# Kernel tuning notes

Measured on AMD Instinct MI355X. Metric: run time of the kernel, lower is better.

The kernel has to match this reference:

```python
import jax, jax.numpy as jnp
import numpy as np

N_BATCH = 2; N_RAYS = 4096; S_COARSE = 32; S_FINE = 32
FEATURE_DIM = 32; BOX_WARP = 6.0; EPS = 1e-5

_PLANE_AXES = np.array([[[1, 0, 0], [0, 1, 0], [0, 0, 1]],
                        [[1, 0, 0], [0, 0, 1], [0, 1, 0]],
                        [[0, 0, 1], [0, 1, 0], [1, 0, 0]]], dtype=np.float32)
_INV_PLANES = np.linalg.inv(_PLANE_AXES)  # [3,3,3]


def _grid_sample(feat, coords):
    # feat [B,C,H,W], coords [B,M,2] in [-1,1] (x->W, y->H); bilinear, align_corners=False, zero padding
    B, C, H, W = feat.shape
    x = (coords[..., 0] + 1.0) * (W * 0.5) - 0.5
    y = (coords[..., 1] + 1.0) * (H * 0.5) - 0.5
    x0 = jnp.floor(x); y0 = jnp.floor(y)
    wx = x - x0; wy = y - y0
    x0i = x0.astype(jnp.int32); y0i = y0.astype(jnp.int32)

    def corner(fb, yi, xi):
        valid = ((xi >= 0) & (xi < W) & (yi >= 0) & (yi < H)).astype(fb.dtype)
        v = fb[:, jnp.clip(yi, 0, H - 1), jnp.clip(xi, 0, W - 1)]  # [C,M]
        return v * valid[None, :]

    def one(fb, x0b, y0b, wxb, wyb):
        x1b = x0b + 1; y1b = y0b + 1
        return (corner(fb, y0b, x0b) * (1 - wxb) * (1 - wyb)
                + corner(fb, y0b, x1b) * wxb * (1 - wyb)
                + corner(fb, y1b, x0b) * (1 - wxb) * wyb
                + corner(fb, y1b, x1b) * wxb * wyb)  # [C,M]

    return jax.vmap(one)(feat, x0i, y0i, wx, wy)  # [B,C,M]


def _sample_from_planes(planes, coords):
    # planes [N,3,C,H,W], coords [N,M,3] -> [N,3,M,C]
    N, n_planes, C, H, W = planes.shape
    M = coords.shape[1]
    c = coords * (2.0 / BOX_WARP)
    proj = jnp.einsum('nmc,pcd->npmd', c, jnp.asarray(_INV_PLANES))[..., :2]  # [N,3,M,2]
    out = _grid_sample(planes.reshape(N * n_planes, C, H, W), proj.reshape(N * n_planes, M, 2))
    return out.reshape(N, n_planes, C, M).transpose(0, 1, 3, 2)


def _decoder(feat, W1, b1, W2, b2):
    # OSGDecoder: Linear -> softplus -> Linear; rgb sigmoid-squashed, sigma raw
    h = jax.nn.softplus(feat @ W1 + b1)
    o = h @ W2 + b2
    rgb = jax.nn.sigmoid(o[..., 1:]) * (1 + 2 * 0.001) - 0.001
    sigma = o[..., 0:1]
    return rgb, sigma


def _run_model(planes, coords, W1, b1, W2, b2, beta):
    sf = _sample_from_planes(planes, coords).mean(axis=1)  # [N,M,C]
    rgb, raw_sigma = _decoder(sf, W1, b1, W2, b2)
    pred_sdf = raw_sigma
    # template SDF stand-in (external FLAME tex_feature net): sphere SDF
    tsdf = jnp.linalg.norm(coords, axis=-1, keepdims=True) - 0.5
    sigma = raw_sigma + tsdf
    density = jax.nn.sigmoid(-sigma / beta) / beta  # sdf_activation(-sigma)
    return rgb, density, pred_sdf


def _ray_march(colors, densities, depths):
    deltas = depths[:, :, 1:] - depths[:, :, :-1]
    c_mid = 0.5 * (colors[:, :, :-1] + colors[:, :, 1:])
    d_mid = 0.5 * (densities[:, :, :-1] + densities[:, :, 1:])
    z_mid = 0.5 * (depths[:, :, :-1] + depths[:, :, 1:])
    alpha = 1.0 - jnp.exp(-d_mid * deltas)
    shifted = jnp.concatenate([jnp.ones_like(alpha[:, :, :1]), 1.0 - alpha + 1e-10], axis=2)
    weights = alpha * jnp.cumprod(shifted, axis=2)[:, :, :-1]
    comp_rgb = jnp.sum(weights * c_mid, axis=2) * 2.0 - 1.0
    w_tot = jnp.sum(weights, axis=2)
    comp_depth = jnp.sum(weights * z_mid, axis=2) / w_tot
    comp_depth = jnp.nan_to_num(comp_depth, nan=jnp.inf)
    comp_depth = jnp.clip(comp_depth, depths.min(), depths.max())
    return comp_rgb, comp_depth, weights


def _sample_pdf(bins, weights, u):
    n_w = weights.shape[-1]
    w = weights + EPS
    pdf = w / jnp.sum(w, axis=-1, keepdims=True)
    cdf = jnp.cumsum(pdf, axis=-1)
    cdf = jnp.concatenate([jnp.zeros_like(cdf[:, :1]), cdf], axis=-1)
    inds = jax.vmap(lambda c, uu: jnp.searchsorted(c, uu, side='right'))(cdf, u)
    below = jnp.maximum(inds - 1, 0)
    above = jnp.minimum(inds, n_w)
    cdf0 = jnp.take_along_axis(cdf, below, axis=-1)
    cdf1 = jnp.take_along_axis(cdf, above, axis=-1)
    b0 = jnp.take_along_axis(bins, below, axis=-1)
    b1v = jnp.take_along_axis(bins, above, axis=-1)
    denom = cdf1 - cdf0
    denom = jnp.where(denom < EPS, 1.0, denom)
    return b0 + (u - cdf0) / denom * (b1v - b0)


def _sample_importance(z_vals, weights, u):
    B, R, S, _ = z_vals.shape
    z = z_vals.reshape(B * R, S)
    w = weights.reshape(B * R, -1)  # S-1
    # torch max_pool1d(k=2,s=1,pad=1) then avg_pool1d(k=2,s=1)
    neg = jnp.full_like(w[:, :1], -1e10)
    wp = jnp.concatenate([neg, w, neg], axis=-1)
    m = jnp.maximum(wp[:, :-1], wp[:, 1:])  # len S
    w_sm = 0.5 * (m[:, :-1] + m[:, 1:]) + 0.01  # len S-1
    z_mid = 0.5 * (z[:, :-1] + z[:, 1:])  # len S-1
    s = _sample_pdf(z_mid, w_sm[:, 1:-1], u)
    return jax.lax.stop_gradient(s.reshape(B, R, -1, 1))


def reference(planes, ray_origins, ray_directions, hit_min_depth, hit_max_depth, jitter, u_importance, W1, b1, W2, b2, sigmoid_beta, hit_mask):
    N, M, _ = ray_origins.shape
    beta = jnp.maximum(sigmoid_beta, 0.002)
    mask = hit_mask.astype(planes.dtype)[:, :, None, None]  # [N,M,1,1]
    hmin = jnp.where(mask == 0, hit_min_depth.min(), hit_min_depth)
    hmax = jnp.where(mask == 0, hit_max_depth.max(), hit_max_depth)
    base = jnp.linspace(0.0, 1.0, S_COARSE, dtype=planes.dtype).reshape(1, 1, S_COARSE, 1)
    span = hmax - hmin
    d_coarse = (base + jitter * span / S_COARSE) * span + hmin  # [N,M,S,1]

    def eval_points(depths):
        coords = ray_origins[:, :, None, :] + depths * ray_directions[:, :, None, :]
        S = depths.shape[2]
        rgb, dens, psdf = _run_model(planes, coords.reshape(N, M * S, 3), W1, b1, W2, b2, beta)
        # masked scatter-back into dense buffers == multiply by hit mask
        rgb = rgb.reshape(N, M, S, FEATURE_DIM) * mask
        dens = dens.reshape(N, M, S, 1) * mask
        return rgb, dens, psdf

    rgb_c, dens_c, psdf_c = eval_points(d_coarse)
    _, _, w_c = _ray_march(rgb_c, dens_c, d_coarse)
    d_fine = _sample_importance(d_coarse, w_c, u_importance)
    rgb_f, dens_f, psdf_f = eval_points(d_fine)

    all_d = jnp.concatenate([d_coarse, d_fine], axis=2)
    all_c = jnp.concatenate([rgb_c, rgb_f], axis=2)
    all_s = jnp.concatenate([dens_c, dens_f], axis=2)
    idx = jnp.argsort(all_d, axis=2)
    all_d = jnp.take_along_axis(all_d, idx, axis=2)
    all_c = jnp.take_along_axis(all_c, jnp.broadcast_to(idx, all_c.shape), axis=2)
    all_s = jnp.take_along_axis(all_s, jnp.broadcast_to(idx, all_s.shape), axis=2)

    rgb_final, depth_final, weights = _ray_march(all_c, all_s, all_d)
    all_pred_sdf = jnp.concatenate([psdf_c, psdf_f], axis=1)
    return rgb_final, depth_final, weights, all_pred_sdf


def setup_inputs():
    key = jax.random.key(0)
    ks = jax.random.split(key, 12)
    planes = jax.random.normal(ks[0], (N_BATCH, 3, 32, 256, 256), jnp.float32)
    ray_origins = 0.1 * jax.random.normal(ks[1], (N_BATCH, N_RAYS, 3), jnp.float32)
    rd = jax.random.normal(ks[2], (N_BATCH, N_RAYS, 3), jnp.float32)
    ray_directions = rd / jnp.linalg.norm(rd, axis=-1, keepdims=True)
    hit_min_depth = 0.8 + 0.4 * jax.random.uniform(ks[3], (N_BATCH, N_RAYS, 1, 1), jnp.float32)
    hit_max_depth = hit_min_depth + 0.5 + jax.random.uniform(ks[4], (N_BATCH, N_RAYS, 1, 1), jnp.float32)
    jitter = jax.random.uniform(ks[5], (N_BATCH, N_RAYS, S_COARSE, 1), jnp.float32)
    u_importance = jax.random.uniform(ks[6], (N_BATCH * N_RAYS, S_FINE), jnp.float32)
    W1 = 0.05 * jax.random.normal(ks[7], (32, 64), jnp.float32)
    b1 = jnp.zeros((64,), jnp.float32)
    W2 = 0.05 * jax.random.normal(ks[8], (64, 1 + FEATURE_DIM), jnp.float32)
    b2 = jnp.zeros((1 + FEATURE_DIM,), jnp.float32)
    sigmoid_beta = 0.1 * jnp.ones((1,), jnp.float32)
    hit_mask = jax.random.randint(ks[9], (N_BATCH, N_RAYS), 0, 2, jnp.int32)
    return {'planes': planes, 'ray_origins': ray_origins, 'ray_directions': ray_directions,
            'hit_min_depth': hit_min_depth, 'hit_max_depth': hit_max_depth, 'jitter': jitter,
            'u_importance': u_importance, 'W1': W1, 'b1': b1, 'W2': W2, 'b2': b2,
            'sigmoid_beta': sigmoid_beta, 'hit_mask': hit_mask}
```

## Files before the change

### kernel.cpp

```cpp
#include <hip/hip_runtime.h>
#include <hip/hip_bf16.h>
#include <math.h>
#include <stddef.h>

typedef unsigned int u32;
typedef unsigned short u16;
typedef unsigned long long u64;

#define NRAYS 8192
#define NSAMP 262144

__device__ __forceinline__ float fa(float a,float b){ return __fadd_rn(a,b); }
__device__ __forceinline__ float fs(float a,float b){ return __fsub_rn(a,b); }
__device__ __forceinline__ float fm(float a,float b){ return __fmul_rn(a,b); }
__device__ __forceinline__ float fdv(float a,float b){ return __fdiv_rn(a,b); }

__device__ __forceinline__ double exp_d(double x){
  const double LOG2E  = 1.4426950408889634074;
  const double LN2_HI = 6.93147180369123816490e-01;
  const double LN2_LO = 1.90821492927058770002e-10;
  double kd = rint(x * LOG2E);
  if (kd >  200.0) return INFINITY;
  if (kd < -200.0) return 0.0;
  int k = (int)kd;
  double r = fma(-kd, LN2_HI, x);
  r = fma(-kd, LN2_LO, r);
  double p = 1.0/39916800.0;
  p = fma(p, r, 1.0/3628800.0);
  p = fma(p, r, 1.0/362880.0);
  p = fma(p, r, 1.0/40320.0);
  p = fma(p, r, 1.0/5040.0);
  p = fma(p, r, 1.0/720.0);
  p = fma(p, r, 1.0/120.0);
  p = fma(p, r, 1.0/24.0);
  p = fma(p, r, 1.0/6.0);
  p = fma(p, r, 0.5);
  p = fma(p, r, 1.0);
  p = fma(p, r, 1.0);
  u64 sb = ((u64)(k + 1023)) << 52;
  return p * __longlong_as_double((long long)sb);
}
__device__ __forceinline__ float exf(float x){ return (float)exp_d((double)x); }
__device__ __forceinline__ float sigm(float x){
  if (x >= 0.f){ float e = exf(-x); return fdv(1.f, fa(1.f, e)); }
  float e = exf(x); return fdv(e, fa(1.f, e));
}
__device__ __forceinline__ float sigm_fast(float x){
  return 1.f/(1.f + __expf(-x));
}
__device__ __forceinline__ u16 f2b(float f){
  u32 x = __float_as_uint(f);
  return (u16)((x + 0x7fffu + ((x>>16)&1u)) >> 16);
}
__device__ __forceinline__ u32 fenc(float f){ u32 b=__float_as_uint(f); return (b&0x80000000u)? ~b : (b|0x80000000u); }
__device__ __forceinline__ float fdec(u32 k){ u32 b=(k&0x80000000u)? (k^0x80000000u) : ~k; return __uint_as_float(b); }

__global__ void k_init(const float* __restrict__ hmin, const float* __restrict__ hmax,
                       const float* __restrict__ W1, float* __restrict__ scal,
                       float* __restrict__ W1t){
  __shared__ float smn[256], smx[256];
  int t = threadIdx.x;
  float mn = 1e30f, mx = -1e30f;
  for (int i=t;i<NRAYS;i+=256){ mn=fminf(mn,hmin[i]); mx=fmaxf(mx,hmax[i]); }
  smn[t]=mn; smx[t]=mx; __syncthreads();
  for(int s=128;s>0;s>>=1){
    if(t<s){ smn[t]=fminf(smn[t],smn[t+s]); smx[t]=fmaxf(smx[t],smx[t+s]); }
    __syncthreads();
  }
  if(t==0){
    scal[0]=smn[0]; scal[1]=smx[0];
    ((u32*)scal)[2]=0xFFFFFFFFu;
    ((u32*)scal)[3]=0u;
  }
  for(int i=t;i<2048;i+=256){ int j=i>>5, c=i&31; W1t[i]=W1[c*64+j]; }
}

__global__ void __launch_bounds__(256) k_tr(const float* __restrict__ pl, float* __restrict__ pt){
  int t = blockIdx.x*256 + threadIdx.x;
  int x  = t & 255;
  int c4 = ((t>>8)&7)<<2;
  int y  = (t>>11)&255;
  int np = t>>19;
  const float* ip = pl + (((size_t)(np*32+c4))<<16) + (y<<8) + x;
  float4 o;
  o.x = ip[0];
  o.y = ip[65536];
  o.z = ip[131072];
  o.w = ip[196608];
  *reinterpret_cast<float4*>(pt + ((((size_t)(np<<8|y))<<8|x)<<5) + c4) = o;
}

template<int PHASE>
__global__ void __launch_bounds__(256) k_eval(
  const float* __restrict__ pt, const float* __restrict__ ro, const float* __restrict__ rd,
  const float* __restrict__ hmin, const float* __restrict__ hmax,
  const float* __restrict__ jitter, const int* __restrict__ hitmask,
  const float* __restrict__ W1t, const float* __restrict__ b1,
  const float* __restrict__ W2, const float* __restrict__ b2,
  const float* __restrict__ sb, float* __restrict__ scal,
  float* __restrict__ dep, float* __restrict__ dens_out, u16* __restrict__ rgb_out,
  float* __restrict__ out_psdf)
{
  __shared__ float sfeat[4][64][33];
  int tid = threadIdx.x;
  int wid = tid>>6, lane = tid&63;
  int blockbase = blockIdx.x*256;
  int idx = blockbase + tid;
  int ray = idx >> 5;
  int s   = idx & 31;
  int n   = ray >> 12;
  int msk = hitmask[ray];

  float d;
  if (PHASE==0){
    float hmn = msk ? hmin[ray] : scal[0];
    float hmx = msk ? hmax[ray] : scal[1];
    float span = fs(hmx, hmn);
    float jit  = jitter[idx];
    float base = (float)((double)s * (1.0/31.0));
    if (s==31) base = 1.0f;
    float t1 = fdv(fm(jit, span), 32.0f);
    d = fa(fm(fa(base, t1), span), hmn);
    dep[idx] = d;
    float dm=d, dM=d;
#pragma unroll
    for (int m=1;m<64;m<<=1){ dm=fminf(dm,__shfl_xor(dm,m)); dM=fmaxf(dM,__shfl_xor(dM,m)); }
    if ((tid & 63)==0){
      atomicMin(((u32*)scal)+2, fenc(dm));
      atomicMax(((u32*)scal)+3, fenc(dM));
    }
  } else {
    d = dep[idx];
  }

  float tsdf, cxo, cyo, czo;
  {
    const float sc2 = (float)(2.0/6.0);
    float ox=ro[ray*3+0], oy=ro[ray*3+1], oz=ro[ray*3+2];
    float dx=rd[ray*3+0], dy=rd[ray*3+1], dz=rd[ray*3+2];
    float px = fa(ox, fm(d,dx)), py = fa(oy, fm(d,dy)), pz = fa(oz, fm(d,dz));
    float nrm = __fsqrt_rn(fa(fa(fm(px,px),fm(py,py)),fm(pz,pz)));
    tsdf = fs(nrm, 0.5f);
    cxo = fm(px,sc2);
    cyo = fm(py,sc2);
    czo = fm(pz,sc2);
  }

  int pg = lane >> 3;
  int q  = lane & 7;
#pragma unroll 2
  for (int r=0;r<8;r++){
    int pidx = r*8 + pg;
    int n2   = ((blockbase + (wid<<6) + pidx) >> 17);
    float cx = __shfl(cxo, pidx);
    float cy = __shfl(cyo, pidx);
    float cz = __shfl(czo, pidx);

    float fchunk[4];
#pragma unroll
    for(int i=0;i<4;i++) fchunk[i]=0.f;

#pragma unroll
    for (int p=0;p<3;p++){
      float u = (p==2)?cz:cx;
      float v = (p==1)?cz:cy;
      float fx = fs(fm(fa(u,1.f),128.f),0.5f);
      float fy = fs(fm(fa(v,1.f),128.f),0.5f);
      float x0f = floorf(fx), y0f = floorf(fy);
      float wx = fs(fx,x0f), wy = fs(fy,y0f);
      float ax0 = fs(1.f,wx), ax1 = wx, ay0 = fs(1.f,wy), ay1 = wy;
      int x0, y0;
      {
        x0 = (x0f >= 2.1e9f) ? 2147483647 : ((x0f <= -2.1e9f) ? (-2147483647-1) : (int)x0f);
        y0 = (y0f >= 2.1e9f) ? 2147483647 : ((y0f <= -2.1e9f) ? (-2147483647-1) : (int)y0f);
      }
      int x1=x0+1, y1=y0+1;
      bool vx0 = (x0>=0 && x0<256), vx1 = (x1>=0 && x1<256);
      bool vy0 = (y0>=0 && y0<256), vy1 = (y1>=0 && y1<256);
      bool ok00 = vx0&&vy0, ok01 = vx1&&vy0, ok10 = vx0&&vy1, ok11 = vx1&&vy1;
      int cx0=min(max(x0,0),255), cx1=min(max(x1,0),255);
      int cy0=min(max(y0,0),255), cy1=min(max(y1,0),255);
      size_t pb = ((size_t)(n2*3+p))<<16;
      int qo = q<<2;
      const float4* t00 = (const float4*)(pt + ((pb + (cy0<<8) + cx0)<<5) + qo);
      const float4* t01 = (const float4*)(pt + ((pb + (cy0<<8) + cx1)<<5) + qo);
      const float4* t10 = (const float4*)(pt + ((pb + (cy1<<8) + cx0)<<5) + qo);
      const float4* t11 = (const float4*)(pt + ((pb + (cy1<<8) + cx1)<<5) + qo);
      float4 v00 = *t00, v01 = *t01, v10 = *t10, v11 = *t11;
      float e0,e1,e2,e3, t_;
#define CORNER_SUM(FLD, OUTI) \
      e0 = ok00 ? v00.FLD : 0.f; e1 = ok01 ? v01.FLD : 0.f; \
      e2 = ok10 ? v10.FLD : 0.f; e3 = ok11 ? v11.FLD : 0.f; \
      t_ = fa(fa(fa(fm(fm(e0,ax0),ay0), fm(fm(e1,ax1),ay0)), fm(fm(e2,ax0),ay1)), fm(fm(e3,ax1),ay1)); \
      fchunk[OUTI] = fa(fchunk[OUTI], t_);
      CORNER_SUM(x,0) CORNER_SUM(y,1) CORNER_SUM(z,2) CORNER_SUM(w,3)
#undef CORNER_SUM
    }
#pragma unroll
    for(int i=0;i<4;i++)
      sfeat[wid][pidx][q*4+i] = fdv(fchunk[i], 3.0f);
  }
  __syncthreads();

  float feat[32];
#pragma unroll
  for(int c=0;c<32;c++) feat[c] = sfeat[wid][lane][c];

  float o[33];
#pragma unroll
  for(int k=0;k<33;k++) o[k]=0.f;
#pragma unroll 2
  for(int j=0;j<64;j++){
    float a = 0.f;
#pragma unroll
    for(int c=0;c<32;c++) a = fmaf(feat[c], W1t[j*32+c], a);
    a = fa(a, b1[j]);
    float h = fa(fmaxf(a,0.f), __logf(fa(1.f, __expf(-fabsf(a)))));
#pragma unroll
    for(int k=0;k<33;k++) o[k] = fmaf(h, W2[j*33+k], o[k]);
  }
#pragma unroll
  for(int k=0;k<33;k++) o[k] = fa(o[k], b2[k]);

  float beta = fmaxf(sb[0], 0.002f);
  float raw = o[0];
  out_psdf[((size_t)n<<18) + ((size_t)PHASE<<17) + (size_t)(ray&4095)*32 + s] = raw;
  float sg = fa(raw, tsdf);
  float dens = msk ? fdv(sigm(fdv(-sg, beta)), beta) : 0.f;
  dens_out[idx]=dens;

  u16 rv[32];
#pragma unroll
  for(int c=0;c<32;c++){
    float r = msk ? fs(fm(sigm_fast(o[c+1]), 1.002f), 0.001f) : 0.f;
    rv[c]=f2b(r);
  }
  uint4* op = (uint4*)(rgb_out + (size_t)idx*32);
#pragma unroll
  for(int q2=0;q2<4;q2++){
    uint4 w;
    w.x = (u32)rv[q2*8+0] | ((u32)rv[q2*8+1]<<16);
    w.y = (u32)rv[q2*8+2] | ((u32)rv[q2*8+3]<<16);
    w.z = (u32)rv[q2*8+4] | ((u32)rv[q2*8+5]<<16);
    w.w = (u32)rv[q2*8+6] | ((u32)rv[q2*8+7]<<16);
    op[q2]=w;
  }
}

__global__ void __launch_bounds__(64) k_imp(
  const float* __restrict__ dc, const float* __restrict__ dens,
  const float* __restrict__ u_imp, float* __restrict__ df, float* __restrict__ scal)
{
  __shared__ float scdf[64][30];
  __shared__ float szm [64][30];
  int tid = threadIdx.x;
  int ray = blockIdx.x*64 + tid;
  float w[31];
  float dprev = dc[ray*32+0];
  float sprev = dens[ray*32+0];
  float T = 1.f;
#pragma unroll
  for(int i=0;i<31;i++){
    float dn = dc[ray*32+i+1];
    float sn = dens[ray*32+i+1];
    if (i<30) szm[tid][i] = fm(0.5f, fa(dprev,dn));
    float delta = fs(dn,dprev);
    float dm = fm(0.5f, fa(sprev,sn));
    float al = fs(1.f, exf(-fm(dm,delta)));
    w[i] = fm(al,T);
    T = fm(T, fa(fs(1.f,al), 1e-10f));
    dprev=dn; sprev=sn;
  }
  float pdfw[29];
#pragma unroll
  for(int i=0;i<29;i++){
    float m1 = fmaxf(w[i],w[i+1]), m2 = fmaxf(w[i+1],w[i+2]);
    pdfw[i] = fa(fa(fm(0.5f, fa(m1,m2)), 0.01f), 1e-5f);
  }
  float sum;
  {
    float r[8];
#pragma unroll
    for(int j=0;j<8;j++) r[j]=pdfw[j];
#pragma unroll
    for(int j=0;j<8;j++) r[j]=fa(r[j],pdfw[8+j]);
#pragma unroll
    for(int j=0;j<8;j++) r[j]=fa(r[j],pdfw[16+j]);
    sum = fa(fa(fa(r[0],r[1]),fa(r[2],r[3])), fa(fa(r[4],r[5]),fa(r[6],r[7])));
#pragma unroll
    for(int i=24;i<29;i++) sum = fa(sum, pdfw[i]);
  }
  {
    float cacc = 0.f;
    scdf[tid][0] = 0.f;
#pragma unroll
    for(int i=1;i<30;i++){
      cacc = fa(cacc, fdv(pdfw[i-1], sum));
      scdf[tid][i] = cacc;
    }
  }

  float fmn=1e30f, fmx=-1e30f;
  for(int k=0;k<32;k++){
    float u = u_imp[ray*32+k];
    int lo=0, hi=30;
    while(lo<hi){
      int mid=(lo+hi)>>1;
      if (scdf[tid][mid] <= u) lo = mid+1; else hi = mid;
    }
    int ind = lo;
    int below = ind-1;
    int above = (ind>29)?29:ind;
    float cdf0 = scdf[tid][below];
    float cdf1 = scdf[tid][above];
    float b0   = szm [tid][below];
    float b1v  = szm [tid][above];
    float den = fs(cdf1,cdf0);
    if((double)den < 1e-5) den = 1.f;
    float sres = fa(b0, fm(fdv(fs(u,cdf0),den), fs(b1v,b0)));
    df[ray*32+k]=sres;
    fmn=fminf(fmn,sres); fmx=fmaxf(fmx,sres);
  }
#pragma unroll
  for(int m=1;m<64;m<<=1){ fmn=fminf(fmn,__shfl_xor(fmn,m)); fmx=fmaxf(fmx,__shfl_xor(fmx,m)); }
  if(tid==0){
    atomicMin(((u32*)scal)+2, fenc(fmn));
    atomicMax(((u32*)scal)+3, fenc(fmx));
  }
}

__global__ void __launch_bounds__(256) k_final(
  const float* __restrict__ dc, const float* __restrict__ df,
  const float* __restrict__ densc, const float* __restrict__ densf,
  const u16* __restrict__ rgbc, const u16* __restrict__ rgbf,
  const float* __restrict__ scal,
  float* __restrict__ out_rgb, float* __restrict__ out_depth, float* __restrict__ out_w)
{
  __shared__ float ssd[4][64];
  __shared__ float ssn[4][64];
  __shared__ int   sp [4][64];
  __shared__ float swv[4][64];
  __shared__ float swz[4][64];
  int wid = threadIdx.x>>6, lane = threadIdx.x&63;
  int ray = blockIdx.x*4 + wid;

  float myd = (lane<32)? dc[ray*32+lane]    : df[ray*32+lane-32];
  float myn = (lane<32)? densc[ray*32+lane] : densf[ray*32+lane-32];
  ssd[wid][lane]=myd; __syncthreads();
  int rk=0;
#pragma unroll 8
  for(int j=0;j<64;j++){
    float dj = ssd[wid][j];
    rk += (dj<myd || (dj==myd && j<lane)) ? 1:0;
  }
  __syncthreads();
  ssd[wid][rk]=myd; ssn[wid][rk]=myn; sp[wid][rk]=lane;
  __syncthreads();

  float T=1.f, accr=0.f;
  int j0 = sp[wid][0];
  float cprev = 0.f;
  if (lane<32){
    const u16* cb = (j0<32)? (rgbc+((size_t)ray*32+j0)*32) : (rgbf+((size_t)ray*32+(j0-32))*32);
    cprev = __uint_as_float(((u32)cb[lane])<<16);
  }
  float d0 = ssd[wid][0], n0 = ssn[wid][0];
  for(int s2=0;s2<63;s2++){
    float d1 = ssd[wid][s2+1], n1 = ssn[wid][s2+1];
    float delta = fs(d1,d0);
    float dm = fm(0.5f, fa(n0,n1));
    float al = fs(1.f, exf(-fm(dm,delta)));
    float wv = fm(al,T);
    T = fm(T, fa(fs(1.f,al), 1e-10f));
    if (lane==s2){ swv[wid][s2]=wv; swz[wid][s2]=fm(wv, fm(0.5f, fa(d0,d1))); }
    int j1 = sp[wid][s2+1];
    float cnext = 0.f;
    if (lane<32){
      const u16* cb = (j1<32)? (rgbc+((size_t)ray*32+j1)*32) : (rgbf+((size_t)ray*32+(j1-32))*32);
      cnext = __uint_as_float(((u32)cb[lane])<<16);
    }
    accr = fa(accr, fm(wv, fm(0.5f, fa(cprev,cnext))));
    cprev=cnext; d0=d1; n0=n1;
  }
  __syncthreads();
  if(lane<63) out_w[(size_t)ray*63+lane]=swv[wid][lane];
  if(lane<32) out_rgb[(size_t)ray*32+lane]=fs(fm(accr,2.f),1.f);
  if(lane==0){
    float wsum, zsum;
    {
      float r[8], rz[8];
#pragma unroll
      for(int j=0;j<8;j++){ r[j]=swv[wid][j]; rz[j]=swz[wid][j]; }
      for(int i=8;i<56;i+=8)
#pragma unroll
        for(int j=0;j<8;j++){ r[j]=fa(r[j],swv[wid][i+j]); rz[j]=fa(rz[j],swz[wid][i+j]); }
      wsum = fa(fa(fa(r[0],r[1]),fa(r[2],r[3])), fa(fa(r[4],r[5]),fa(r[6],r[7])));
      zsum = fa(fa(fa(rz[0],rz[1]),fa(rz[2],rz[3])), fa(fa(rz[4],rz[5]),fa(rz[6],rz[7])));
      for(int i=56;i<63;i++){ wsum=fa(wsum,swv[wid][i]); zsum=fa(zsum,swz[wid][i]); }
    }
    float depv = fdv(zsum, wsum);
    if (isnan(depv)) depv = INFINITY;
    float lo = fdec(((const u32*)scal)[2]);
    float hi = fdec(((const u32*)scal)[3]);
    depv = fminf(fmaxf(depv,lo),hi);
    out_depth[ray]=depv;
  }
}

extern "C" void kernel_launch(void* const* d_in, const int* in_sizes, int n_in,
                              void* d_out, int out_size, void* d_ws, size_t ws_size,
                              hipStream_t stream) {
  const float* planes = (const float*)d_in[0];
  const float* ro     = (const float*)d_in[1];
  const float* rdp    = (const float*)d_in[2];
  const float* hmin   = (const float*)d_in[3];
  const float* hmax   = (const float*)d_in[4];
  const float* jitter = (const float*)d_in[5];
  const float* uimp   = (const float*)d_in[6];
  const float* W1     = (const float*)d_in[7];
  const float* b1     = (const float*)d_in[8];
  const float* W2     = (const float*)d_in[9];
  const float* b2     = (const float*)d_in[10];
  const float* sb     = (const float*)d_in[11];
  const int*   hmk    = (const int*)d_in[12];
  float* out = (float*)d_out;
  char* ws = (char*)d_ws;

  size_t off=0;
  auto alloc=[&](size_t bytes){ size_t o=off; off=(off+bytes+255)&~(size_t)255; return o; };
  float* scal = (float*)(ws+alloc(64));
  float* W1t  = (float*)(ws+alloc(2048*4));
  float* pt   = (float*)(ws+alloc((size_t)12582912*4));
  float* dco  = (float*)(ws+alloc((size_t)NSAMP*4));
  float* dfi  = (float*)(ws+alloc((size_t)NSAMP*4));
  float* dnc  = (float*)(ws+alloc((size_t)NSAMP*4));
  float* dnf  = (float*)(ws+alloc((size_t)NSAMP*4));
  u16*   rgc  = (u16*)  (ws+alloc((size_t)NSAMP*32*2));
  u16*   rgf  = (u16*)  (ws+alloc((size_t)NSAMP*32*2));
  (void)in_sizes; (void)n_in; (void)out_size; (void)ws_size;

  float* out_rgb  = out;
  float* out_dep  = out + 262144;
  float* out_w    = out + 270336;
  float* out_psdf = out + 786432;

  k_init<<<dim3(1),dim3(256),0,stream>>>(hmin,hmax,W1,scal,W1t);
  k_tr<<<dim3(12288),dim3(256),0,stream>>>(planes, pt);
  k_eval<0><<<dim3(1024),dim3(256),0,stream>>>(pt,ro,rdp,hmin,hmax,jitter,hmk,W1t,b1,W2,b2,sb,scal,dco,dnc,rgc,out_psdf);
  k_imp<<<dim3(128),dim3(64),0,stream>>>(dco,dnc,uimp,dfi,scal);
  k_eval<1><<<dim3(1024),dim3(256),0,stream>>>(pt,ro,rdp,hmin,hmax,jitter,hmk,W1t,b1,W2,b2,sb,scal,dfi,dnf,rgf,out_psdf);
  k_final<<<dim3(2048),dim3(256),0,stream>>>(dco,dfi,dnc,dnf,rgc,rgf,scal,out_rgb,out_dep,out_w);
}
```

Measured before the change: 418.4 us.

## Split eval blocks so all four waves gather features for half the samples

Each 256-thread block now handles 128 samples instead of 256. All four waves share the bilinear triplane gathering through shared-memory coordinates, and only the first two waves run the MLP decoder. The grid doubles to cover every sample. The aim is more parallelism on the memory-bound gather phase, at the cost of half the threads idling during the MLP and an extra barrier.

```diff
diff --git a/kernel.cpp b/kernel.cpp
--- a/kernel.cpp
+++ b/kernel.cpp
@@ -101,60 +101,60 @@
   float* __restrict__ dep, float* __restrict__ dens_out, u16* __restrict__ rgb_out,
   float* __restrict__ out_psdf)
 {
-  __shared__ float sfeat[4][64][33];
+  __shared__ float sfeat[128][33];
+  __shared__ float scrd [3][128];
   int tid = threadIdx.x;
   int wid = tid>>6, lane = tid&63;
-  int blockbase = blockIdx.x*256;
+  int blockbase = blockIdx.x*128;
   int idx = blockbase + tid;
   int ray = idx >> 5;
   int s   = idx & 31;
-  int n   = ray >> 12;
-  int msk = hitmask[ray];
-
-  float d;
-  if (PHASE==0){
-    float hmn = msk ? hmin[ray] : scal[0];
-    float hmx = msk ? hmax[ray] : scal[1];
-    float span = fs(hmx, hmn);
-    float jit  = jitter[idx];
-    float base = (float)((double)s * (1.0/31.0));
-    if (s==31) base = 1.0f;
-    float t1 = fdv(fm(jit, span), 32.0f);
-    d = fa(fm(fa(base, t1), span), hmn);
-    dep[idx] = d;
-    float dm=d, dM=d;
-#pragma unroll
-    for (int m=1;m<64;m<<=1){ dm=fminf(dm,__shfl_xor(dm,m)); dM=fmaxf(dM,__shfl_xor(dM,m)); }
-    if ((tid & 63)==0){
-      atomicMin(((u32*)scal)+2, fenc(dm));
-      atomicMax(((u32*)scal)+3, fenc(dM));
-    }
-  } else {
-    d = dep[idx];
-  }
-
-  float tsdf, cxo, cyo, czo;
-  {
+  int n   = blockbase >> 17;
+  int msk = 0;
+
+  float d = 0.f, tsdf = 0.f;
+  if (tid < 128){
+    msk = hitmask[ray];
+    if (PHASE==0){
+      float hmn = msk ? hmin[ray] : scal[0];
+      float hmx = msk ? hmax[ray] : scal[1];
+      float span = fs(hmx, hmn);
+      float jit  = jitter[idx];
+      float base = (float)((double)s * (1.0/31.0));
+      if (s==31) base = 1.0f;
+      float t1 = fdv(fm(jit, span), 32.0f);
+      d = fa(fm(fa(base, t1), span), hmn);
+      dep[idx] = d;
+      float dm=d, dM=d;
+#pragma unroll
+      for (int m=1;m<64;m<<=1){ dm=fminf(dm,__shfl_xor(dm,m)); dM=fmaxf(dM,__shfl_xor(dM,m)); }
+      if (lane==0){
+        atomicMin(((u32*)scal)+2, fenc(dm));
+        atomicMax(((u32*)scal)+3, fenc(dM));
+      }
+    } else {
+      d = dep[idx];
+    }
     const float sc2 = (float)(2.0/6.0);
     float ox=ro[ray*3+0], oy=ro[ray*3+1], oz=ro[ray*3+2];
     float dx=rd[ray*3+0], dy=rd[ray*3+1], dz=rd[ray*3+2];
     float px = fa(ox, fm(d,dx)), py = fa(oy, fm(d,dy)), pz = fa(oz, fm(d,dz));
     float nrm = __fsqrt_rn(fa(fa(fm(px,px),fm(py,py)),fm(pz,pz)));
     tsdf = fs(nrm, 0.5f);
-    cxo = fm(px,sc2);
-    cyo = fm(py,sc2);
-    czo = fm(pz,sc2);
-  }
+    scrd[0][tid] = fm(px,sc2);
+    scrd[1][tid] = fm(py,sc2);
+    scrd[2][tid] = fm(pz,sc2);
+  }
+  __syncthreads();
 
   int pg = lane >> 3;
   int q  = lane & 7;
 #pragma unroll 2
-  for (int r=0;r<8;r++){
-    int pidx = r*8 + pg;
-    int n2   = ((blockbase + (wid<<6) + pidx) >> 17);
-    float cx = __shfl(cxo, pidx);
-    float cy = __shfl(cyo, pidx);
-    float cz = __shfl(czo, pidx);
+  for (int r=0;r<4;r++){
+    int pidx = (wid*4 + r)*8 + pg;
+    float cx = scrd[0][pidx];
+    float cy = scrd[1][pidx];
+    float cz = scrd[2][pidx];
 
     float fchunk[4];
 #pragma unroll
@@ -180,7 +180,7 @@
       bool ok00 = vx0&&vy0, ok01 = vx1&&vy0, ok10 = vx0&&vy1, ok11 = vx1&&vy1;
       int cx0=min(max(x0,0),255), cx1=min(max(x1,0),255);
       int cy0=min(max(y0,0),255), cy1=min(max(y1,0),255);
-      size_t pb = ((size_t)(n2*3+p))<<16;
+      size_t pb = ((size_t)(n*3+p))<<16;
       int qo = q<<2;
       const float4* t00 = (const float4*)(pt + ((pb + (cy0<<8) + cx0)<<5) + qo);
       const float4* t01 = (const float4*)(pt + ((pb + (cy0<<8) + cx1)<<5) + qo);
@@ -198,13 +198,15 @@
     }
 #pragma unroll
     for(int i=0;i<4;i++)
-      sfeat[wid][pidx][q*4+i] = fdv(fchunk[i], 3.0f);
+      sfeat[pidx][q*4+i] = fdv(fchunk[i], 3.0f);
   }
   __syncthreads();
 
+  if (tid >= 128) return;
+
   float feat[32];
 #pragma unroll
-  for(int c=0;c<32;c++) feat[c] = sfeat[wid][lane][c];
+  for(int c=0;c<32;c++) feat[c] = sfeat[tid][c];
 
   float o[33];
 #pragma unroll
@@ -446,8 +448,8 @@
 
   k_init<<<dim3(1),dim3(256),0,stream>>>(hmin,hmax,W1,scal,W1t);
   k_tr<<<dim3(12288),dim3(256),0,stream>>>(planes, pt);
-  k_eval<0><<<dim3(1024),dim3(256),0,stream>>>(pt,ro,rdp,hmin,hmax,jitter,hmk,W1t,b1,W2,b2,sb,scal,dco,dnc,rgc,out_psdf);
+  k_eval<0><<<dim3(2048),dim3(256),0,stream>>>(pt,ro,rdp,hmin,hmax,jitter,hmk,W1t,b1,W2,b2,sb,scal,dco,dnc,rgc,out_psdf);
   k_imp<<<dim3(128),dim3(64),0,stream>>>(dco,dnc,uimp,dfi,scal);
-  k_eval<1><<<dim3(1024),dim3(256),0,stream>>>(pt,ro,rdp,hmin,hmax,jitter,hmk,W1t,b1,W2,b2,sb,scal,dfi,dnf,rgf,out_psdf);
+  k_eval<1><<<dim3(2048),dim3(256),0,stream>>>(pt,ro,rdp,hmin,hmax,jitter,hmk,W1t,b1,W2,b2,sb,scal,dfi,dnf,rgf,out_psdf);
   k_final<<<dim3(2048),dim3(256),0,stream>>>(dco,dfi,dnc,dnf,rgc,rgf,scal,out_rgb,out_dep,out_w);
 }
```

Result: slower. 432.9 us (+3.5%).
